# Kernel tuning notes

Measured on AMD Instinct MI355X. Metric: run time of the kernel, lower is better.

The kernel has to match this reference:

```python
import jax, jax.numpy as jnp
import numpy as np

THETA = 10000.0

def _rope_cache(seq_len, d_k, dtype=jnp.float32):
    # theta_k = theta ** (-(2i/d_k)), angles[n, i] = n * theta_k[i]
    inv_freq = THETA ** (-(jnp.arange(0, d_k, 2, dtype=jnp.float32) / d_k))
    pos = jnp.arange(seq_len, dtype=jnp.float32)
    ang = pos[:, None] * inv_freq[None, :]          # [S, d_k/2]
    cos = jnp.repeat(jnp.cos(ang), 2, axis=-1)      # [S, d_k]
    sin = jnp.repeat(jnp.sin(ang), 2, axis=-1)
    return cos.astype(dtype), sin.astype(dtype)

def _apply_rope(x, cos, sin):
    # x: [..., S, d_k]; rotate even/odd pairs: rot[2i] = -x[2i+1], rot[2i+1] = x[2i]
    x2 = x.reshape(x.shape[:-1] + (x.shape[-1] // 2, 2))
    rot = jnp.stack([-x2[..., 1], x2[..., 0]], axis=-1).reshape(x.shape)
    return x * cos + rot * sin

def setup_inputs() -> dict:
    key = jax.random.key(0)
    ks = jax.random.split(key, 5)
    B, S, D = 2, 2048, 1024
    H, DK = 16, 64
    scale = (2.0 / (D + DK)) ** 0.5
    x = jax.random.normal(ks[0], (B, S, D), dtype=jnp.float32)
    Wq = jax.random.normal(ks[1], (H, D, DK), dtype=jnp.float32) * scale
    Wk = jax.random.normal(ks[2], (H, D, DK), dtype=jnp.float32) * scale
    Wv = jax.random.normal(ks[3], (H, D, DK), dtype=jnp.float32) * scale
    Wo = jax.random.normal(ks[4], (D, D), dtype=jnp.float32) * (2.0 / (2 * D)) ** 0.5
    return {"x": x, "Wq": Wq, "Wk": Wk, "Wv": Wv, "Wo": Wo}

def reference(x, Wq, Wk, Wv, Wo):
    B, S, D = x.shape
    H, _, DK = Wq.shape
    cos, sin = _rope_cache(S, DK, x.dtype)          # [S, DK]
    q = jnp.einsum('bsd,hdk->bhsk', x, Wq)
    k = jnp.einsum('bsd,hdk->bhsk', x, Wk)
    v = jnp.einsum('bsd,hdk->bhsk', x, Wv)
    q = _apply_rope(q, cos, sin)
    k = _apply_rope(k, cos, sin)
    scores = jnp.einsum('bhqk,bhsk->bhqs', q, k) / jnp.sqrt(jnp.asarray(DK, x.dtype))
    causal = jnp.tril(jnp.ones((S, S), dtype=bool))
    scores = jnp.where(causal, scores, -jnp.inf)
    attn = jax.nn.softmax(scores, axis=-1)
    out = jnp.einsum('bhqs,bhsk->bhqk', attn, v)    # [B,H,S,DK]
    out = out.transpose(0, 2, 1, 3).reshape(B, S, H * DK)  # concat heads
    return jnp.einsum('bsd,do->bso', out, Wo)
```

## Files before the change

### kernel.cpp

```cpp
#include <hip/hip_runtime.h>
#include <math.h>

typedef __attribute__((ext_vector_type(8))) short bf16x8;
typedef __attribute__((ext_vector_type(4))) float f32x4;
typedef __attribute__((ext_vector_type(16))) float f32x16;
typedef __attribute__((ext_vector_type(4))) unsigned int uint32x4;
typedef __attribute__((ext_vector_type(2))) unsigned int uint32x2;
typedef unsigned short ushort_t;
typedef unsigned int uint_t;

typedef const void __attribute__((address_space(1)))* gas_ptr;
typedef void __attribute__((address_space(3)))* las_ptr;

namespace {

constexpr int S_  = 2048;
constexpr int D_  = 1024;
constexpr float CSC = 0.18033688011f;

__device__ inline ushort_t f2bf(float f) {
    uint_t u = __builtin_bit_cast(uint_t, f);
    u += 0x7FFFu + ((u >> 16) & 1u);
    return (ushort_t)(u >> 16);
}
__device__ inline uint_t cvtpk(float lo, float hi) {
    uint_t r;
    asm("v_cvt_pk_bf16_f32 %0, %1, %2" : "=v"(r) : "v"(lo), "v"(hi));
    return r;
}
__device__ inline void plswap(uint_t& d, uint_t& s) {
    uint32x2 r = __builtin_amdgcn_permlane32_swap(d, s, false, false);
    d = r[0];
    s = r[1];
}
__device__ inline float xhalf_sum(float x) {
    uint_t d = __builtin_bit_cast(uint_t, x), s = d;
    plswap(d, s);
    return __builtin_bit_cast(float, d) + __builtin_bit_cast(float, s);
}

__device__ inline void tconv_body(const float* __restrict__ src,
                                  ushort_t* __restrict__ dst,
                                  int R, int C, int r0, int c0, int tid)
{
    __shared__ float Tl[64][65];
    #pragma unroll
    for (int l = 0; l < 4; ++l) {
        int i = tid + l * 256;
        int row = i >> 4, col = (i & 15) * 4;
        float4 v = *(const float4*)(src + (size_t)(r0 + row) * C + c0 + col);
        Tl[row][col] = v.x; Tl[row][col + 1] = v.y;
        Tl[row][col + 2] = v.z; Tl[row][col + 3] = v.w;
    }
    __syncthreads();
    #pragma unroll
    for (int l = 0; l < 4; ++l) {
        int i = tid + l * 256;
        int cc = i >> 4, rr = (i & 15) * 4;
        uint_t lo = (uint_t)f2bf(Tl[rr][cc])     | ((uint_t)f2bf(Tl[rr + 1][cc]) << 16);
        uint_t hi = (uint_t)f2bf(Tl[rr + 2][cc]) | ((uint_t)f2bf(Tl[rr + 3][cc]) << 16);
        *(uint2*)(dst + (size_t)(c0 + cc) * R + r0 + rr) = make_uint2(lo, hi);
    }
}

__global__ __launch_bounds__(256)
void prep_kernel(const float* __restrict__ x,  const float* __restrict__ Wq,
                 const float* __restrict__ Wk, const float* __restrict__ Wv,
                 const float* __restrict__ Wo,
                 ushort_t* __restrict__ xb, ushort_t* __restrict__ Wt,
                 ushort_t* __restrict__ Wot, float* __restrict__ tbl)
{
    const int b = blockIdx.x, tid = threadIdx.x;
    if (b < 2048) {
        int i = b * 256 + tid;
        float4 a = ((const float4*)x)[i * 2];
        float4 c = ((const float4*)x)[i * 2 + 1];
        uint_t u0 = (uint_t)f2bf(a.x) | ((uint_t)f2bf(a.y) << 16);
        uint_t u1 = (uint_t)f2bf(a.z) | ((uint_t)f2bf(a.w) << 16);
        uint_t u2 = (uint_t)f2bf(c.x) | ((uint_t)f2bf(c.y) << 16);
        uint_t u3 = (uint_t)f2bf(c.z) | ((uint_t)f2bf(c.w) << 16);
        ((uint4*)xb)[i] = make_uint4(u0, u1, u2, u3);
    } else if (b < 2304) {
        int i = (b - 2048) * 256 + tid;
        int s = i >> 5, p = i & 31;
        float inv = powf(10000.0f, -(float)p * (1.0f / 32.0f));
        float sn, cs;
        sincosf((float)s * inv, &sn, &cs);
        ((float2*)tbl)[i] = make_float2(cs, sn);
    } else if (b < 3072) {
        int lin = b - 2304;
        int z = lin >> 4, rx = lin & 15;
        const float* src = (z < 16 ? Wq : z < 32 ? Wk : Wv) + (size_t)(z & 15) * 65536;
        tconv_body(src, Wt + (size_t)z * 65536, 1024, 64, rx * 64, 0, tid);
    } else {
        int lin = b - 3072;
        tconv_body(Wo, Wot, 1024, 1024, (lin & 15) * 64, (lin >> 4) * 64, tid);
    }
}

__global__ __launch_bounds__(256)
void gemm_kernel(const ushort_t* __restrict__ A, const ushort_t* __restrict__ Bt,
                 ushort_t* __restrict__ Qo, ushort_t* __restrict__ Ko,
                 ushort_t* __restrict__ Vto,
                 const float* __restrict__ tbl, int K)
{
    __shared__ char smem[34816];
    ushort_t* As = (ushort_t*)smem;
    ushort_t* Bs = As + 4096;

    const int tid  = threadIdx.x;
    const int w    = tid >> 6, lane = tid & 63;
    const int lq   = lane & 15, lk = lane >> 4;
    const int wr   = w >> 1, wc = w & 1;
    const int m0   = blockIdx.x * 128;
    const int n0   = blockIdx.y * 128;

    f32x4 acc[4][4] = {};

    for (int k0 = 0; k0 < K; k0 += 32) {
        #pragma unroll
        for (int i = 0; i < 2; ++i) {
            int c   = i * 256 + tid;
            int row = c >> 2, c4 = c & 3;
            const ushort_t* ga = A  + (size_t)(m0 + row) * K + k0 + c4 * 8;
            const ushort_t* gb = Bt + (size_t)(n0 + row) * K + k0 + c4 * 8;
            int base = (i * 256 + w * 64) * 16;
            __builtin_amdgcn_global_load_lds((gas_ptr)ga, (las_ptr)((char*)As + base), 16, 0, 0);
            __builtin_amdgcn_global_load_lds((gas_ptr)gb, (las_ptr)((char*)Bs + base), 16, 0, 0);
        }
        __syncthreads();

        bf16x8 a[4], b[4];
        #pragma unroll
        for (int m = 0; m < 4; ++m)
            a[m] = *(const bf16x8*)((const char*)As + (wr * 64 + m * 16 + lq) * 64 + lk * 16);
        #pragma unroll
        for (int n = 0; n < 4; ++n)
            b[n] = *(const bf16x8*)((const char*)Bs + (wc * 64 + n * 16 + lq) * 64 + lk * 16);
        #pragma unroll
        for (int m = 0; m < 4; ++m)
            #pragma unroll
            for (int n = 0; n < 4; ++n)
                acc[m][n] = __builtin_amdgcn_mfma_f32_16x16x32_bf16(a[m], b[n], acc[m][n], 0, 0, 0);
        __syncthreads();
    }

    const int sel = n0 >> 10;
    ushort_t* EP = (ushort_t*)smem;
    const int h0 = (n0 & 1023) >> 6;
    if (sel < 2) {
        const float sc = (sel == 0) ? CSC : 1.0f;
        #pragma unroll
        for (int m = 0; m < 4; ++m) {
            #pragma unroll
            for (int r = 0; r < 4; ++r) {
                int lrow = wr * 64 + m * 16 + lk * 4 + r;
                int sG = (m0 + lrow) & 2047;
                #pragma unroll
                for (int n = 0; n < 4; ++n) {
                    int lcol = wc * 64 + n * 16 + lq;
                    int dk = lcol & 63;
                    float v = acc[m][n][r] * sc;
                    float2 cs = *(const float2*)(tbl + ((size_t)sG * 32 + (dk >> 1)) * 2);
                    float sp = __shfl_xor(v, 1);
                    float rv = (dk & 1) ? (v * cs.x + sp * cs.y)
                                        : (v * cs.x - sp * cs.y);
                    EP[lrow * 136 + lcol] = f2bf(rv);
                }
            }
        }
        __syncthreads();
        ushort_t* dst = (sel == 0) ? Qo : Ko;
        #pragma unroll
        for (int it = 0; it < 8; ++it) {
            int idx = it * 256 + tid;
            int row = idx >> 4, c16 = idx & 15;
            uint4 v = *(const uint4*)(EP + row * 136 + c16 * 8);
            int mg = m0 + row;
            int b_ = mg >> 11, s = mg & 2047;
            int h = h0 + (c16 >> 3);
            int dk0 = (c16 & 7) * 8;
            *(uint4*)(dst + (((size_t)b_ * 16 + h) * 2048 + s) * 64 + dk0) = v;
        }
    } else {
        #pragma unroll
        for (int m = 0; m < 4; ++m) {
            #pragma unroll
            for (int r = 0; r < 4; ++r) {
                int lrow = wr * 64 + m * 16 + lk * 4 + r;
                #pragma unroll
                for (int n = 0; n < 4; ++n) {
                    int lcol = wc * 64 + n * 16 + lq;
                    EP[lcol * 136 + lrow] = f2bf(acc[m][n][r]);
                }
            }
        }
        __syncthreads();
        #pragma unroll
        for (int it = 0; it < 8; ++it) {
            int idx = it * 256 + tid;
            int col = idx >> 4, c16 = idx & 15;
            uint4 v = *(const uint4*)(EP + col * 136 + c16 * 8);
            int h = h0 + (col >> 6);
            int dk = col & 63;
            int sb = m0 + c16 * 8;
            int b_ = sb >> 11, s = sb & 2047;
            *(uint4*)(Vto + (((size_t)b_ * 16 + h) * 64 + dk) * 2048 + s) = v;
        }
    }
}

__global__ __launch_bounds__(256)
void gemm2_kernel(const ushort_t* __restrict__ A, const ushort_t* __restrict__ Bt,
                  float* __restrict__ Co, int K)
{
    __shared__ char smem[17408];
    ushort_t* As = (ushort_t*)smem;
    ushort_t* Bs = As + 2048;

    const int tid = threadIdx.x;
    const int w = tid >> 6, lane = tid & 63;
    const int lq = lane & 15, lk = lane >> 4;
    const int wr = w >> 1, wc = w & 1;
    const int m0 = blockIdx.x * 64;
    const int n0 = blockIdx.y * 128;

    f32x4 acc[2][4] = {};

    for (int k0 = 0; k0 < K; k0 += 32) {
        {
            int slot = tid;
            int row = slot >> 2, c4 = slot & 3;
            const ushort_t* ga = A + (size_t)(m0 + row) * K + k0 + c4 * 8;
            __builtin_amdgcn_global_load_lds((gas_ptr)ga, (las_ptr)((char*)As + (w * 64 + lane) * 16), 16, 0, 0);
        }
        #pragma unroll
        for (int i = 0; i < 2; ++i) {
            int slot = i * 256 + tid;
            int row = slot >> 2, c4 = slot & 3;
            const ushort_t* gb = Bt + (size_t)(n0 + row) * K + k0 + c4 * 8;
            int base = (i * 256 + w * 64) * 16;
            __builtin_amdgcn_global_load_lds((gas_ptr)gb, (las_ptr)((char*)Bs + base), 16, 0, 0);
        }
        __syncthreads();

        bf16x8 a[2], b[4];
        #pragma unroll
        for (int m = 0; m < 2; ++m)
            a[m] = *(const bf16x8*)((const char*)As + (wr * 32 + m * 16 + lq) * 64 + lk * 16);
        #pragma unroll
        for (int n = 0; n < 4; ++n)
            b[n] = *(const bf16x8*)((const char*)Bs + (wc * 64 + n * 16 + lq) * 64 + lk * 16);
        #pragma unroll
        for (int m = 0; m < 2; ++m)
            #pragma unroll
            for (int n = 0; n < 4; ++n)
                acc[m][n] = __builtin_amdgcn_mfma_f32_16x16x32_bf16(a[m], b[n], acc[m][n], 0, 0, 0);
        __syncthreads();
    }

    float* EPf = (float*)smem;
    #pragma unroll
    for (int c = 0; c < 2; ++c) {
        __syncthreads();
        if (wr == c) {
            #pragma unroll
            for (int m = 0; m < 2; ++m)
                #pragma unroll
                for (int r = 0; r < 4; ++r) {
                    int lrow = m * 16 + lk * 4 + r;
                    #pragma unroll
                    for (int n = 0; n < 4; ++n) {
                        int lcol = wc * 64 + n * 16 + lq;
                        EPf[lrow * 132 + lcol] = acc[m][n][r];
                    }
                }
        }
        __syncthreads();
        #pragma unroll
        for (int it = 0; it < 4; ++it) {
            int idx = it * 256 + tid;
            int rl = idx >> 5, c32 = idx & 31;
            float4 v = *(const float4*)(EPf + rl * 132 + c32 * 4);
            *(float4*)(Co + (size_t)(m0 + c * 32 + rl) * D_ + n0 + c32 * 4) = v;
        }
    }
}

__global__ __launch_bounds__(512)
void attn_kernel(const ushort_t* __restrict__ Q, const ushort_t* __restrict__ Kg,
                 const ushort_t* __restrict__ Vt, ushort_t* __restrict__ O)
{
    __shared__ ushort_t Ks[2][128 * 64];
    __shared__ ushort_t Vs[2][64 * 128];

    const int bid = blockIdx.x;
    const int p  = 31 - (bid >> 5);
    const int bh = bid & 31;

    const int tid = threadIdx.x;
    const int w = tid >> 6, lane = tid & 63;
    const int wq = w & 1, st = w >> 1;
    const int lq = lane & 31, hi = lane >> 5;
    const size_t bhBase = (size_t)bh * S_ * 64;

    const int nt   = (p >> 1) + 1;
    const int qrel = ((p & 1) << 1) + wq;

    bf16x8 qf[4];
    {
        const ushort_t* qp = Q + bhBase + (size_t)(p * 64 + wq * 32 + lq) * 64 + hi * 8;
        qf[0] = *(const bf16x8*)(qp);
        qf[1] = *(const bf16x8*)(qp + 16);
        qf[2] = *(const bf16x8*)(qp + 32);
        qf[3] = *(const bf16x8*)(qp + 48);
    }

    const int slot0 = tid, slot1 = 512 + tid;
    const int rK0 = slot0 >> 3, rK1 = slot1 >> 3;
    const int rV0 = slot0 >> 4, rV1 = slot1 >> 4;
    const ushort_t* gk0 = Kg + bhBase + (size_t)rK0 * 64 + ((slot0 & 7) ^ (rK0 & 7)) * 8;
    const ushort_t* gk1 = Kg + bhBase + (size_t)rK1 * 64 + ((slot1 & 7) ^ (rK1 & 7)) * 8;
    const ushort_t* gv0 = Vt + bhBase + (size_t)rV0 * 2048 + ((slot0 & 15) ^ (rV0 & 7)) * 8;
    const ushort_t* gv1 = Vt + bhBase + (size_t)rV1 * 2048 + ((slot1 & 15) ^ (rV1 & 7)) * 8;

    auto stage = [&](int buf, int t) {
        const size_t ko = (size_t)t * 128 * 64;
        const size_t vo = (size_t)t * 128;
        __builtin_amdgcn_global_load_lds((gas_ptr)(gk0 + ko), (las_ptr)((char*)Ks[buf] + slot0 * 16), 16, 0, 0);
        __builtin_amdgcn_global_load_lds((gas_ptr)(gk1 + ko), (las_ptr)((char*)Ks[buf] + slot1 * 16), 16, 0, 0);
        __builtin_amdgcn_global_load_lds((gas_ptr)(gv0 + vo), (las_ptr)((char*)Vs[buf] + slot0 * 16), 16, 0, 0);
        __builtin_amdgcn_global_load_lds((gas_ptr)(gv1 + vo), (las_ptr)((char*)Vs[buf] + slot1 * 16), 16, 0, 0);
    };

    float l = 0.0f;
    f32x16 oacc[2] = {};

    const int krow = st * 32 + lq;

    stage(0, 0);

    for (int t = 0; t < nt; ++t) {
        const int cur = t & 1;
        if (t < nt - 1) {
            stage(cur ^ 1, t + 1);
            asm volatile("s_waitcnt vmcnt(4)" ::: "memory");
        } else {
            asm volatile("s_waitcnt vmcnt(0)" ::: "memory");
        }
        __builtin_amdgcn_s_barrier();
        asm volatile("" ::: "memory");

        const bool last = (t == nt - 1);
        if (!(last && st > qrel)) {
            f32x16 sacc = {};
            #pragma unroll
            for (int c = 0; c < 4; ++c) {
                int koff = krow * 128 + ((c * 32 + hi * 16) ^ ((krow & 7) << 4));
                bf16x8 kf = *(const bf16x8*)((const char*)Ks[cur] + koff);
                sacc = __builtin_amdgcn_mfma_f32_32x32x16_bf16(kf, qf[c], sacc, 0, 0, 0);
            }

            if (last && st == qrel) {
                #pragma unroll
                for (int idx = 0; idx < 16; ++idx) {
                    int kvl = (idx & 3) + 8 * (idx >> 2) + 4 * hi;
                    if (kvl > lq) sacc[idx] = -1e30f;
                }
            }

            float pv[16];
            #pragma unroll
            for (int idx = 0; idx < 16; ++idx) {
                float v = exp2f(sacc[idx] - 32.0f);
                pv[idx] = v;
                l += v;
            }

            #pragma unroll
            for (int c2 = 0; c2 < 2; ++c2) {
                uint_t w0 = cvtpk(pv[8 * c2 + 0], pv[8 * c2 + 1]);
                uint_t w1 = cvtpk(pv[8 * c2 + 2], pv[8 * c2 + 3]);
                uint_t w2 = cvtpk(pv[8 * c2 + 4], pv[8 * c2 + 5]);
                uint_t w3 = cvtpk(pv[8 * c2 + 6], pv[8 * c2 + 7]);
                plswap(w0, w2);
                plswap(w1, w3);
                uint32x4 pw; pw[0] = w0; pw[1] = w1; pw[2] = w2; pw[3] = w3;
                bf16x8 pb = __builtin_bit_cast(bf16x8, pw);
                #pragma unroll
                for (int d2 = 0; d2 < 2; ++d2) {
                    int vrow = d2 * 32 + lq;
                    int vslot = (st * 4 + c2 * 2 + hi) ^ (vrow & 7);
                    bf16x8 vf = *(const bf16x8*)((const char*)Vs[cur] + vrow * 256 + vslot * 16);
                    oacc[d2] = __builtin_amdgcn_mfma_f32_32x32x16_bf16(vf, pb, oacc[d2], 0, 0, 0);
                }
            }
        }
        asm volatile("" ::: "memory");
        __builtin_amdgcn_s_barrier();
        asm volatile("" ::: "memory");
    }

    l = xhalf_sum(l);

    __syncthreads();

    float* ksf = (float*)Ks;
    float* vsf = (float*)Vs;
    const int rowi = wq * 64 + lane;
    vsf[st * 128 + rowi] = l;
    if (st == 3) {
        #pragma unroll
        for (int j = 0; j < 8; ++j) {
            f32x4 v4;
            v4[0] = oacc[j >> 2][(j & 3) * 4 + 0];
            v4[1] = oacc[j >> 2][(j & 3) * 4 + 1];
            v4[2] = oacc[j >> 2][(j & 3) * 4 + 2];
            v4[3] = oacc[j >> 2][(j & 3) * 4 + 3];
            *(f32x4*)(ksf + rowi * 32 + ((j ^ (rowi & 7)) * 4)) = v4;
        }
    }
    __syncthreads();
    if (st == 2) {
        #pragma unroll
        for (int j = 0; j < 8; ++j) {
            int soff = rowi * 32 + ((j ^ (rowi & 7)) * 4);
            f32x4 v4 = *(const f32x4*)(ksf + soff);
            v4[0] += oacc[j >> 2][(j & 3) * 4 + 0];
            v4[1] += oacc[j >> 2][(j & 3) * 4 + 1];
            v4[2] += oacc[j >> 2][(j & 3) * 4 + 2];
            v4[3] += oacc[j >> 2][(j & 3) * 4 + 3];
            *(f32x4*)(ksf + soff) = v4;
        }
    }
    __syncthreads();
    if (st == 1) {
        #pragma unroll
        for (int j = 0; j < 8; ++j) {
            int soff = rowi * 32 + ((j ^ (rowi & 7)) * 4);
            f32x4 v4 = *(const f32x4*)(ksf + soff);
            v4[0] += oacc[j >> 2][(j & 3) * 4 + 0];
            v4[1] += oacc[j >> 2][(j & 3) * 4 + 1];
            v4[2] += oacc[j >> 2][(j & 3) * 4 + 2];
            v4[3] += oacc[j >> 2][(j & 3) * 4 + 3];
            *(f32x4*)(ksf + soff) = v4;
        }
    }
    __syncthreads();
    if (st == 0) {
        float lt = vsf[rowi] + vsf[128 + rowi] + vsf[256 + rowi] + vsf[384 + rowi];
        float inv = 1.0f / lt;
        const int b_ = bh >> 4, h = bh & 15;
        const int s = p * 64 + wq * 32 + lq;
        ushort_t* ob = O + ((size_t)b_ * 2048 + s) * 1024 + h * 64;
        #pragma unroll
        for (int j = 0; j < 8; ++j) {
            int soff = rowi * 32 + ((j ^ (rowi & 7)) * 4);
            f32x4 v4 = *(const f32x4*)(ksf + soff);
            int d2 = j >> 2, base = (j & 3) * 4;
            float q0 = (oacc[d2][base + 0] + v4[0]) * inv;
            float q1 = (oacc[d2][base + 1] + v4[1]) * inv;
            float q2 = (oacc[d2][base + 2] + v4[2]) * inv;
            float q3 = (oacc[d2][base + 3] + v4[3]) * inv;
            uint2 pkv;
            pkv.x = cvtpk(q0, q1);
            pkv.y = cvtpk(q2, q3);
            *(uint2*)(ob + d2 * 32 + 8 * (j & 3) + 4 * hi) = pkv;
        }
    }
}

}

extern "C" void kernel_launch(void* const* d_in, const int* in_sizes, int n_in,
                              void* d_out, int out_size, void* d_ws, size_t ws_size,
                              hipStream_t stream)
{
    const float* x  = (const float*)d_in[0];
    const float* Wq = (const float*)d_in[1];
    const float* Wk = (const float*)d_in[2];
    const float* Wv = (const float*)d_in[3];
    const float* Wo = (const float*)d_in[4];

    ushort_t* xb  = (ushort_t*)d_ws;
    ushort_t* Wt  = xb  + 4194304;
    ushort_t* Wot = Wt  + 3145728;
    ushort_t* Qb  = Wot + 1048576;
    ushort_t* Kb  = Qb  + 4194304;
    ushort_t* Vtb = Kb  + 4194304;
    ushort_t* Ob  = Vtb + 4194304;
    float*    tbl = (float*)(Ob + 4194304);

    prep_kernel<<<3328, 256, 0, stream>>>(x, Wq, Wk, Wv, Wo, xb, Wt, Wot, tbl);

    gemm_kernel<<<dim3(32, 24), 256, 0, stream>>>(xb, Wt, Qb, Kb, Vtb, tbl, 1024);

    attn_kernel<<<1024, 512, 0, stream>>>(Qb, Kb, Vtb, Ob);

    gemm2_kernel<<<dim3(64, 8), 256, 0, stream>>>(Ob, Wot, (float*)d_out, 1024);
}
```

Baseline: 115.9 us.

## Double-buffer LDS tiles in projection GEMM K-loop with async global-to-LDS loads

The GEMM K-loop now uses two LDS buffers. It issues the global_load_lds for tile t+1 before computing on tile t, and uses explicit s_waitcnt vmcnt and s_barrier instead of __syncthreads. This is meant to hide global-memory latency behind the MFMA work instead of stalling at each iteration. It doubles LDS use for the staging tiles. It also adds a per-lane offset to the LDS pointer, which should be wave-uniform, and that is a correctness risk.

```diff
diff --git a/kernel.cpp b/kernel.cpp
--- a/kernel.cpp
+++ b/kernel.cpp
@@ -105,8 +105,6 @@
                  const float* __restrict__ tbl, int K)
 {
     __shared__ char smem[34816];
-    ushort_t* As = (ushort_t*)smem;
-    ushort_t* Bs = As + 4096;
 
     const int tid  = threadIdx.x;
     const int w    = tid >> 6, lane = tid & 63;
@@ -117,32 +115,59 @@
 
     f32x4 acc[4][4] = {};
 
-    for (int k0 = 0; k0 < K; k0 += 32) {
-        #pragma unroll
-        for (int i = 0; i < 2; ++i) {
-            int c   = i * 256 + tid;
-            int row = c >> 2, c4 = c & 3;
-            const ushort_t* ga = A  + (size_t)(m0 + row) * K + k0 + c4 * 8;
-            const ushort_t* gb = Bt + (size_t)(n0 + row) * K + k0 + c4 * 8;
-            int base = (i * 256 + w * 64) * 16;
-            __builtin_amdgcn_global_load_lds((gas_ptr)ga, (las_ptr)((char*)As + base), 16, 0, 0);
-            __builtin_amdgcn_global_load_lds((gas_ptr)gb, (las_ptr)((char*)Bs + base), 16, 0, 0);
-        }
-        __syncthreads();
-
+    const int c0s  = tid, c1s = 256 + tid;
+    const int row0 = c0s >> 2, cc0 = (c0s & 3) * 8;
+    const int row1 = c1s >> 2, cc1 = (c1s & 3) * 8;
+    const ushort_t* gA0 = A  + (size_t)(m0 + row0) * K + cc0;
+    const ushort_t* gA1 = A  + (size_t)(m0 + row1) * K + cc1;
+    const ushort_t* gB0 = Bt + (size_t)(n0 + row0) * K + cc0;
+    const ushort_t* gB1 = Bt + (size_t)(n0 + row1) * K + cc1;
+    const int l0 = (0 * 256 + w * 64 + lane - w * 64) * 16;
+    const int lds0 = (0 * 256 + w * 64) * 16 + (lane * 16);
+    const int lds1 = (1 * 256 + w * 64) * 16 + (lane * 16);
+    (void)l0;
+
+    auto stage = [&](int buf, int k0) {
+        char* As = smem + buf * 16384;
+        char* Bs = As + 8192;
+        __builtin_amdgcn_global_load_lds((gas_ptr)(gA0 + k0), (las_ptr)(As + lds0), 16, 0, 0);
+        __builtin_amdgcn_global_load_lds((gas_ptr)(gA1 + k0), (las_ptr)(As + lds1), 16, 0, 0);
+        __builtin_amdgcn_global_load_lds((gas_ptr)(gB0 + k0), (las_ptr)(Bs + lds0), 16, 0, 0);
+        __builtin_amdgcn_global_load_lds((gas_ptr)(gB1 + k0), (las_ptr)(Bs + lds1), 16, 0, 0);
+    };
+
+    stage(0, 0);
+
+    const int NT = K >> 5;
+    for (int t = 0; t < NT; ++t) {
+        const int cur = t & 1;
+        if (t < NT - 1) {
+            stage(cur ^ 1, (t + 1) << 5);
+            asm volatile("s_waitcnt vmcnt(4)" ::: "memory");
+        } else {
+            asm volatile("s_waitcnt vmcnt(0)" ::: "memory");
+        }
+        __builtin_amdgcn_s_barrier();
+        asm volatile("" ::: "memory");
+
+        const char* As = smem + cur * 16384;
+        const char* Bs = As + 8192;
         bf16x8 a[4], b[4];
         #pragma unroll
         for (int m = 0; m < 4; ++m)
-            a[m] = *(const bf16x8*)((const char*)As + (wr * 64 + m * 16 + lq) * 64 + lk * 16);
+            a[m] = *(const bf16x8*)(As + (wr * 64 + m * 16 + lq) * 64 + lk * 16);
         #pragma unroll
         for (int n = 0; n < 4; ++n)
-            b[n] = *(const bf16x8*)((const char*)Bs + (wc * 64 + n * 16 + lq) * 64 + lk * 16);
+            b[n] = *(const bf16x8*)(Bs + (wc * 64 + n * 16 + lq) * 64 + lk * 16);
         #pragma unroll
         for (int m = 0; m < 4; ++m)
             #pragma unroll
             for (int n = 0; n < 4; ++n)
                 acc[m][n] = __builtin_amdgcn_mfma_f32_16x16x32_bf16(a[m], b[n], acc[m][n], 0, 0, 0);
-        __syncthreads();
+
+        asm volatile("" ::: "memory");
+        __builtin_amdgcn_s_barrier();
+        asm volatile("" ::: "memory");
     }
 
     const int sel = n0 >> 10;
```

After: 109.3 us. 5.7% less time.
